# Kernel optimization log

Measured on AMD Instinct MI355X. Metric: run time of the kernel, lower is better.

Reference implementation:

```python
import jax, jax.numpy as jnp
import numpy as np

N, E = 100000, 1600000
IN_C, HID, OUT = 128, 64, 25
EPS = 1e-5


def gcn_conv(x, row, col, W, b):
    # PyG GCNConv: h = x@W; add self-loops; sym-norm D^-1/2 A D^-1/2; + bias
    h = x @ W                                   # [N, F]
    ones = jnp.ones(row.shape[0], h.dtype)
    deg = jax.ops.segment_sum(ones, col, num_segments=N) + 1.0  # +1 self-loop
    dinv = jax.lax.rsqrt(deg)                   # [N]
    norm = dinv[row] * dinv[col]                # [E]
    agg = jax.ops.segment_sum(h[row] * norm[:, None], col, num_segments=N)
    agg = agg + (dinv * dinv)[:, None] * h      # self-loop contribution
    return agg + b


def layer_norm(x, w, b):
    # PyG LayerNorm mode='node': normalize each node over feature dim
    mu = jnp.mean(x, axis=-1, keepdims=True)
    var = jnp.var(x, axis=-1, keepdims=True)
    return (x - mu) * jax.lax.rsqrt(var + EPS) * w + b


def setup_inputs() -> dict:
    key = jax.random.key(0)
    ks = jax.random.split(key, 16)
    x = jax.random.normal(ks[0], (N, IN_C), dtype=jnp.float32)
    edge_index = jax.random.randint(ks[1], (2, E), 0, N, dtype=jnp.int32)

    def glorot(k, shp):
        lim = float(np.sqrt(6.0 / (shp[0] + shp[1])))
        return jax.random.uniform(k, shp, jnp.float32, -lim, lim)

    return {
        "x": x,
        "edge_index": edge_index,
        "W1": glorot(ks[2], (IN_C, HID)), "b1": jnp.zeros((HID,), jnp.float32),
        "W2": glorot(ks[3], (HID, HID)), "b2": jnp.zeros((HID,), jnp.float32),
        "W3": glorot(ks[4], (HID, HID)), "b3": jnp.zeros((HID,), jnp.float32),
        "ln1_w": jnp.ones((HID,), jnp.float32), "ln1_b": jnp.zeros((HID,), jnp.float32),
        "ln2_w": jnp.ones((HID,), jnp.float32), "ln2_b": jnp.zeros((HID,), jnp.float32),
        "ln3_w": jnp.ones((HID,), jnp.float32), "ln3_b": jnp.zeros((HID,), jnp.float32),
        "Wl": glorot(ks[5], (HID, OUT)), "bl": jnp.zeros((OUT,), jnp.float32),
    }


def reference(x, edge_index, W1, b1, W2, b2, W3, b3,
              ln1_w, ln1_b, ln2_w, ln2_b, ln3_w, ln3_b, Wl, bl):
    row, col = edge_index[0], edge_index[1]
    h = jax.nn.relu(layer_norm(gcn_conv(x, row, col, W1, b1), ln1_w, ln1_b))
    h = jax.nn.relu(layer_norm(gcn_conv(h, row, col, W2, b2), ln2_w, ln2_b))
    h = jax.nn.relu(layer_norm(gcn_conv(h, row, col, W3, b3), ln3_w, ln3_b))
    pooled = jnp.mean(h, axis=0)                # [HID]
    return pooled @ Wl + bl                     # [OUT]
```

## Files before the change

### kernel.cpp

```cpp
#include <hip/hip_runtime.h>
#include <hip/hip_bf16.h>

typedef __hip_bfloat16 bf16;
typedef __attribute__((ext_vector_type(8))) short short8;
typedef __attribute__((ext_vector_type(4))) float f32x4;
typedef __attribute__((ext_vector_type(2))) float f32x2;

#define HID 64
#define CAP 4096
#define BSH 7
#define EPB 4096

__device__ __forceinline__ unsigned short f2bfbits(float x){
    union { float f; unsigned u; } c; c.f = x;
    unsigned r = c.u + 0x7fffu + ((c.u >> 16) & 1u);
    return (unsigned short)(r >> 16);
}
__device__ __forceinline__ unsigned char f2fp8(float x){
    unsigned v = __builtin_amdgcn_cvt_pk_fp8_f32(x, x, 0u, false);
    return (unsigned char)(v & 0xffu);
}
template<bool HI>
__device__ __forceinline__ f32x2 cvtpk(unsigned u){
    return __builtin_amdgcn_cvt_pk_f32_fp8(u, HI);
}


__global__ __launch_bounds__(1024) void bin_kernel(const int* __restrict__ row,
                                                   const int* __restrict__ col,
                                                   int E, int NB,
                                                   int* __restrict__ gCur,
                                                   int* __restrict__ cnt,
                                                   int* __restrict__ binned,
                                                   unsigned char* __restrict__ H8a,
                                                   unsigned char* __restrict__ H8b,
                                                   int N){
    __shared__ int lCnt[1024];
    __shared__ int lOff[1024];
    __shared__ int lGB[1024];
    __shared__ int sPay[EPB];
    __shared__ unsigned short sB[EPB];
    __shared__ int wSum[16];
    int tid = threadIdx.x;
    int lane = tid & 63, wv = tid >> 6;
    if (blockIdx.x == 0 && tid < 32){
        unsigned* za = (unsigned*)(H8a + ((size_t)N << 6));
        unsigned* zb = (unsigned*)(H8b + ((size_t)N << 6));
        if (tid < 16) za[tid] = 0u; else zb[tid - 16] = 0u;
    }
    int e0 = blockIdx.x * EPB;
    int eN = E - e0; if (eN > EPB) eN = EPB;

    lCnt[tid] = 0;
    int cols[4], rows[4];
    #pragma unroll
    for (int k = 0; k < 4; ++k){
        int i = tid + k * 1024;
        bool ok = (i < eN);
        cols[k] = ok ? col[e0 + i] : -1;
        rows[k] = ok ? row[e0 + i] : 0;
    }
    #pragma unroll
    for (int k = 0; k < 4; ++k)
        if (cols[k] >= 0) atomicAdd(&cnt[cols[k]], 1);
    __syncthreads();
    #pragma unroll
    for (int k = 0; k < 4; ++k)
        if (cols[k] >= 0) atomicAdd(&lCnt[cols[k] >> BSH], 1);
    __syncthreads();

    int c = lCnt[tid];
    int inc = c;
    #pragma unroll
    for (int m = 1; m < 64; m <<= 1){
        int t = __shfl_up(inc, m);
        if (lane >= m) inc += t;
    }
    if (lane == 63) wSum[wv] = inc;
    __syncthreads();
    if (wv == 0 && lane < 16){
        int orig = wSum[lane];
        int ws = orig;
        #pragma unroll
        for (int m = 1; m < 16; m <<= 1){
            int t = __shfl_up(ws, m);
            if (lane >= m) ws += t;
        }
        wSum[lane] = ws - orig;
    }
    __syncthreads();
    int excl = inc - c + wSum[wv];
    lOff[tid] = excl;
    if (c){
        int gb = atomicAdd(&gCur[tid], c);
        lGB[tid] = tid * CAP + gb - excl;
    }
    lCnt[tid] = 0;
    __syncthreads();

    #pragma unroll
    for (int k = 0; k < 4; ++k){
        if (cols[k] >= 0){
            int bk = cols[k] >> BSH;
            int rk = atomicAdd(&lCnt[bk], 1);
            int pos = lOff[bk] + rk;
            sPay[pos] = ((cols[k] & 127) << 17) | rows[k];
            sB[pos] = (unsigned short)bk;
        }
    }
    __syncthreads();

    #pragma unroll
    for (int k = 0; k < 4; ++k){
        int i = tid + k * 1024;
        if (i < eN){
            int bk = sB[i];
            int tgt = lGB[bk] + i;
            if (tgt - (bk << 12) < CAP)
                binned[tgt] = sPay[i];
        }
    }
}


template<int K, typename T>
__global__ __launch_bounds__(256) void matmul_kernel(const T* __restrict__ act,
                                                     const float* __restrict__ W,
                                                     const int* __restrict__ cnt,
                                                     unsigned char* __restrict__ H8, int N){
    constexpr int KS = K / 32;
    constexpr int RB = 2 * K;
    __shared__ __align__(16) short As[128 * K];
    __shared__ __align__(16) short Wt[64 * K];

    int tid = threadIdx.x;
    int nodeBase = blockIdx.x * 128;

    for (int i = tid; i < K * 64; i += 256){
        int k = i >> 6, c = i & 63;
        unsigned short b = f2bfbits(W[i]);
        int byte = c * RB + ((2 * k) ^ ((c & 7) << 4));
        *(short*)((char*)Wt + byte) = (short)b;
    }
    constexpr int OPR = K / 8;
    for (int i = tid; i < 128 * OPR; i += 256){
        int node = i / OPR, oct = i % OPR;
        int n = nodeBase + node;
        short8 v = (short8)0;
        if (n < N){
            if constexpr (sizeof(T) == 4){
                const float4* xp = (const float4*)&act[(size_t)n * K + oct * 8];
                float4 a = xp[0], b = xp[1];
                v[0] = (short)f2bfbits(a.x); v[1] = (short)f2bfbits(a.y);
                v[2] = (short)f2bfbits(a.z); v[3] = (short)f2bfbits(a.w);
                v[4] = (short)f2bfbits(b.x); v[5] = (short)f2bfbits(b.y);
                v[6] = (short)f2bfbits(b.z); v[7] = (short)f2bfbits(b.w);
            } else {
                v = *(const short8*)&act[(size_t)n * K + oct * 8];
            }
        }
        int byte = node * RB + ((oct * 16) ^ ((node & 7) << 4));
        *(short8*)((char*)As + byte) = v;
    }
    __syncthreads();

    int wv = tid >> 6, l = tid & 63;
    int lr = l & 15, lg = l >> 4;

    short8 bfr[KS][4];
    #pragma unroll
    for (int ks = 0; ks < KS; ++ks)
        #pragma unroll
        for (int t = 0; t < 4; ++t){
            int c = t * 16 + lr;
            int byte = c * RB + ((ks * 64 + lg * 16) ^ ((c & 7) << 4));
            bfr[ks][t] = *(const short8*)((const char*)Wt + byte);
        }

    #pragma unroll
    for (int nt = 0; nt < 2; ++nt){
        int nb = wv * 32 + nt * 16;
        int node = nb + lr;
        short8 af[KS];
        #pragma unroll
        for (int ks = 0; ks < KS; ++ks){
            int byte = node * RB + ((ks * 64 + lg * 16) ^ ((node & 7) << 4));
            af[ks] = *(const short8*)((const char*)As + byte);
        }
        f32x4 acc[4] = {(f32x4)0.f, (f32x4)0.f, (f32x4)0.f, (f32x4)0.f};
        #pragma unroll
        for (int ks = 0; ks < KS; ++ks)
            #pragma unroll
            for (int t = 0; t < 4; ++t)
                acc[t] = __builtin_amdgcn_mfma_f32_16x16x32_bf16(af[ks], bfr[ks][t], acc[t], 0, 0, 0);
        #pragma unroll
        for (int r = 0; r < 4; ++r){
            int n = nodeBase + nb + lg * 4 + r;
            if (n < N){
                float dv = rsqrtf((float)cnt[n] + 1.0f);
                #pragma unroll
                for (int t = 0; t < 4; ++t)
                    H8[((size_t)(unsigned)n << 6) + t * 16 + lr] = f2fp8(acc[t][r] * dv);
            }
        }
    }
}


__global__ __launch_bounds__(512) void agg_sort_kernel(const unsigned char* __restrict__ H8in,
                                                       const int* __restrict__ cnt,
                                                       const int* __restrict__ gCur,
                                                       const int* __restrict__ binned,
                                                       int* __restrict__ csr_row,
                                                       int* __restrict__ col_ptr,
                                                       const float* __restrict__ bias,
                                                       const float* __restrict__ lnw,
                                                       const float* __restrict__ lnb,
                                                       const float* __restrict__ Wn,
                                                       unsigned char* __restrict__ H8out,
                                                       int N){
    __shared__ int sCsr[CAP];
    __shared__ __align__(16) short ybuf[8192];
    __shared__ __align__(16) short Wt[4096];
    __shared__ int fineCnt[128];
    __shared__ int fineCur[128];
    __shared__ int sStart[128];
    __shared__ float sdv[128];
    __shared__ int scW[2];
    int b = blockIdx.x, tid = threadIdx.x;
    int wid = tid >> 6, l = tid & 63;
    int g = l >> 2, s = l & 3;
    int nodeBase = b << BSH;
    int n = nodeBase + wid * 16 + g;
    bool valid = (n < N);
    int nc = valid ? n : nodeBase;

    int j0g = b * CAP;
    int cntB = gCur[b];
    if (cntB > CAP) cntB = CAP;

    for (int i = tid; i < 4096; i += 512){
        int k = i >> 6, c = i & 63;
        unsigned short bb = f2bfbits(Wn[i]);
        int byte = c * 128 + ((2 * k) ^ ((c & 7) << 4));
        *(short*)((char*)Wt + byte) = (short)bb;
    }
    if (tid < 128) fineCnt[tid] = 0;
    __syncthreads();

    for (int i = tid; i < cntB; i += 512)
        atomicAdd(&fineCnt[binned[j0g + i] >> 17], 1);
    __syncthreads();

    int cf = 0, inc = 0;
    if (tid < 128){
        cf = fineCnt[tid];
        inc = cf;
        #pragma unroll
        for (int m = 1; m < 64; m <<= 1){
            int t = __shfl_up(inc, m);
            if ((tid & 63) >= m) inc += t;
        }
        if ((tid & 63) == 63) scW[tid >> 6] = inc;
    }
    __syncthreads();
    if (tid < 128){
        int off = (tid >= 64) ? scW[0] : 0;
        int startL = off + inc - cf;
        sStart[tid] = startL;
        fineCur[tid] = startL;
        int node = nodeBase + tid;
        if (node < N) col_ptr[node] = j0g + startL;
    }
    __syncthreads();

    for (int i = tid; i < cntB; i += 512){
        int w = binned[j0g + i];
        int pos = atomicAdd(&fineCur[w >> 17], 1);
        sCsr[pos] = w & 0x1FFFF;
    }
    __syncthreads();
    for (int i = tid; i < cntB; i += 512) csr_row[j0g + i] = sCsr[i];

    int deg = valid ? cnt[nc] : 0;
    int p = sStart[(wid << 4) + g];
    unsigned soff = (unsigned)(s << 4);
    const char* Hb = (const char*)H8in;
    uint4 us = *(const uint4*)(Hb + ((((unsigned)nc) << 6) | soff));

    int mdeg = deg;
    mdeg = max(mdeg, __shfl_xor(mdeg, 4));
    mdeg = max(mdeg, __shfl_xor(mdeg, 8));
    mdeg = max(mdeg, __shfl_xor(mdeg, 16));
    mdeg = max(mdeg, __shfl_xor(mdeg, 32));

    f32x2 a0 = {0.f,0.f}, a1 = {0.f,0.f}, a2 = {0.f,0.f}, a3 = {0.f,0.f};
    f32x2 a4 = {0.f,0.f}, a5 = {0.f,0.f}, a6 = {0.f,0.f}, a7 = {0.f,0.f};
#define ACC4(u) { a0 += cvtpk<false>((u).x); a1 += cvtpk<true>((u).x); \
                  a2 += cvtpk<false>((u).y); a3 += cvtpk<true>((u).y); \
                  a4 += cvtpk<false>((u).z); a5 += cvtpk<true>((u).z); \
                  a6 += cvtpk<false>((u).w); a7 += cvtpk<true>((u).w); }
    for (int i = 0; i < mdeg; i += 4){
        int r0 = (i     < deg) ? sCsr[p + i    ] : N;
        int r1 = (i + 1 < deg) ? sCsr[p + i + 1] : N;
        int r2 = (i + 2 < deg) ? sCsr[p + i + 2] : N;
        int r3 = (i + 3 < deg) ? sCsr[p + i + 3] : N;
        uint4 u0 = *(const uint4*)(Hb + ((((unsigned)r0) << 6) | soff));
        uint4 u1 = *(const uint4*)(Hb + ((((unsigned)r1) << 6) | soff));
        uint4 u2 = *(const uint4*)(Hb + ((((unsigned)r2) << 6) | soff));
        uint4 u3 = *(const uint4*)(Hb + ((((unsigned)r3) << 6) | soff));
        ACC4(u0) ACC4(u1) ACC4(u2) ACC4(u3)
    }
#undef ACC4
    a0 += cvtpk<false>(us.x); a1 += cvtpk<true>(us.x);
    a2 += cvtpk<false>(us.y); a3 += cvtpk<true>(us.y);
    a4 += cvtpk<false>(us.z); a5 += cvtpk<true>(us.z);
    a6 += cvtpk<false>(us.w); a7 += cvtpk<true>(us.w);

    float dv = rsqrtf((float)deg + 1.0f);
    float acc16[16] = { a0.x, a0.y, a1.x, a1.y, a2.x, a2.y, a3.x, a3.y,
                        a4.x, a4.y, a5.x, a5.y, a6.x, a6.y, a7.x, a7.y };
    float v[16], y[16];
    float4 bq[4], wq[4], cq[4];
    #pragma unroll
    for (int q = 0; q < 4; ++q){
        bq[q] = ((const float4*)bias)[(s << 2) + q];
        wq[q] = ((const float4*)lnw)[(s << 2) + q];
        cq[q] = ((const float4*)lnb)[(s << 2) + q];
    }
    #pragma unroll
    for (int j = 0; j < 16; ++j)
        v[j] = fmaf(dv, acc16[j], ((const float*)&bq[j >> 2])[j & 3]);
    float sum = 0.f;
    #pragma unroll
    for (int j = 0; j < 16; ++j) sum += v[j];
    sum += __shfl_xor(sum, 1); sum += __shfl_xor(sum, 2);
    float mu = sum * (1.0f / 64.0f);
    float var = 0.f;
    #pragma unroll
    for (int j = 0; j < 16; ++j){ float d = v[j] - mu; var = fmaf(d, d, var); }
    var += __shfl_xor(var, 1); var += __shfl_xor(var, 2);
    float rstd = rsqrtf(var * (1.0f / 64.0f) + 1e-5f);
    #pragma unroll
    for (int j = 0; j < 16; ++j){
        float d = (v[j] - mu) * rstd;
        y[j] = fmaxf(fmaf(d, ((const float*)&wq[j >> 2])[j & 3],
                             ((const float*)&cq[j >> 2])[j & 3]), 0.0f);
    }

    if (s == 0) sdv[(wid << 4) + g] = dv;
    char* yb = (char*)ybuf;
    int base = (wid << 11) + (g << 7);
    int sw = (g & 7) << 4;
    short8 ya, yz;
    #pragma unroll
    for (int j = 0; j < 8; ++j){ ya[j] = (short)f2bfbits(y[j]); yz[j] = (short)f2bfbits(y[8 + j]); }
    *(short8*)(yb + base + (((s << 5)     ) ^ sw)) = ya;
    *(short8*)(yb + base + (((s << 5) + 16) ^ sw)) = yz;

    int lr = l & 15, lg = l >> 4;
    short8 bfr[2][4];
    #pragma unroll
    for (int ks = 0; ks < 2; ++ks)
        #pragma unroll
        for (int t = 0; t < 4; ++t){
            int c = t * 16 + lr;
            int byte = c * 128 + ((((ks << 2) + lg) << 4) ^ ((c & 7) << 4));
            bfr[ks][t] = *(const short8*)((const char*)Wt + byte);
        }
    short8 af[2];
    #pragma unroll
    for (int ks = 0; ks < 2; ++ks){
        int byte = (wid << 11) + lr * 128 + ((((ks << 2) + lg) << 4) ^ ((lr & 7) << 4));
        af[ks] = *(const short8*)(yb + byte);
    }
    f32x4 acc[4] = {(f32x4)0.f, (f32x4)0.f, (f32x4)0.f, (f32x4)0.f};
    #pragma unroll
    for (int ks = 0; ks < 2; ++ks)
        #pragma unroll
        for (int t = 0; t < 4; ++t)
            acc[t] = __builtin_amdgcn_mfma_f32_16x16x32_bf16(af[ks], bfr[ks][t], acc[t], 0, 0, 0);
    #pragma unroll
    for (int r = 0; r < 4; ++r){
        int nn = nodeBase + (wid << 4) + (lg << 2) + r;
        if (nn < N){
            float dv2 = sdv[(wid << 4) + (lg << 2) + r];
            #pragma unroll
            for (int t = 0; t < 4; ++t)
                H8out[((size_t)(unsigned)nn << 6) + t * 16 + lr] = f2fp8(acc[t][r] * dv2);
        }
    }
}


template<bool POOL>
__global__ __launch_bounds__(256) void agg_kernel(const unsigned char* __restrict__ H8in,
                                                  const int* __restrict__ cnt,
                                                  const int* __restrict__ col_ptr,
                                                  const int* __restrict__ csr_row,
                                                  const float* __restrict__ bias,
                                                  const float* __restrict__ lnw,
                                                  const float* __restrict__ lnb,
                                                  const float* __restrict__ Wn,
                                                  unsigned char* __restrict__ H8out,
                                                  float* __restrict__ pooledRep, int N){
    __shared__ int sIdx[CAP];
    __shared__ __align__(16) short ybuf[POOL ? 8 : 4096];
    __shared__ __align__(16) short Wt[POOL ? 8 : 4096];
    __shared__ float sp[POOL ? 256 : 4];
    __shared__ float sdv[64];
    int tid = threadIdx.x;
    int wid = tid >> 6, l = tid & 63;
    int g = l >> 2, s = l & 3;
    int nodeBase = blockIdx.x * 64;
    int n = nodeBase + wid * 16 + g;
    bool valid = (n < N);
    int nc = valid ? n : nodeBase;

    int lastN = nodeBase + 63; if (lastN > N - 1) lastN = N - 1;
    int jlo = col_ptr[nodeBase];
    int jhi = col_ptr[lastN] + cnt[lastN];
    int cntR = jhi - jlo;

    int deg = valid ? cnt[nc] : 0;
    int p = (valid ? col_ptr[nc] : jlo) - jlo;

    for (int i = tid; i < cntR; i += 256) sIdx[i] = csr_row[jlo + i];
    if (!POOL){
        for (int i = tid; i < 4096; i += 256){
            int k = i >> 6, c = i & 63;
            unsigned short bb = f2bfbits(Wn[i]);
            int byte = c * 128 + ((2 * k) ^ ((c & 7) << 4));
            *(short*)((char*)Wt + byte) = (short)bb;
        }
    }
    __syncthreads();

    unsigned soff = (unsigned)(s << 4);
    const char* Hb = (const char*)H8in;
    uint4 us = *(const uint4*)(Hb + ((((unsigned)nc) << 6) | soff));

    int mdeg = deg;
    mdeg = max(mdeg, __shfl_xor(mdeg, 4));
    mdeg = max(mdeg, __shfl_xor(mdeg, 8));
    mdeg = max(mdeg, __shfl_xor(mdeg, 16));
    mdeg = max(mdeg, __shfl_xor(mdeg, 32));

    f32x2 a0 = {0.f,0.f}, a1 = {0.f,0.f}, a2 = {0.f,0.f}, a3 = {0.f,0.f};
    f32x2 a4 = {0.f,0.f}, a5 = {0.f,0.f}, a6 = {0.f,0.f}, a7 = {0.f,0.f};
#define ACC4(u) { a0 += cvtpk<false>((u).x); a1 += cvtpk<true>((u).x); \
                  a2 += cvtpk<false>((u).y); a3 += cvtpk<true>((u).y); \
                  a4 += cvtpk<false>((u).z); a5 += cvtpk<true>((u).z); \
                  a6 += cvtpk<false>((u).w); a7 += cvtpk<true>((u).w); }
    for (int i = 0; i < mdeg; i += 4){
        int r0 = (i     < deg) ? sIdx[p + i    ] : N;
        int r1 = (i + 1 < deg) ? sIdx[p + i + 1] : N;
        int r2 = (i + 2 < deg) ? sIdx[p + i + 2] : N;
        int r3 = (i + 3 < deg) ? sIdx[p + i + 3] : N;
        uint4 u0 = *(const uint4*)(Hb + ((((unsigned)r0) << 6) | soff));
        uint4 u1 = *(const uint4*)(Hb + ((((unsigned)r1) << 6) | soff));
        uint4 u2 = *(const uint4*)(Hb + ((((unsigned)r2) << 6) | soff));
        uint4 u3 = *(const uint4*)(Hb + ((((unsigned)r3) << 6) | soff));
        ACC4(u0) ACC4(u1) ACC4(u2) ACC4(u3)
    }
#undef ACC4
    a0 += cvtpk<false>(us.x); a1 += cvtpk<true>(us.x);
    a2 += cvtpk<false>(us.y); a3 += cvtpk<true>(us.y);
    a4 += cvtpk<false>(us.z); a5 += cvtpk<true>(us.z);
    a6 += cvtpk<false>(us.w); a7 += cvtpk<true>(us.w);

    float dv = rsqrtf((float)deg + 1.0f);
    float acc16[16] = { a0.x, a0.y, a1.x, a1.y, a2.x, a2.y, a3.x, a3.y,
                        a4.x, a4.y, a5.x, a5.y, a6.x, a6.y, a7.x, a7.y };
    float v[16], y[16];
    float4 bq[4], wq[4], cq[4];
    #pragma unroll
    for (int q = 0; q < 4; ++q){
        bq[q] = ((const float4*)bias)[(s << 2) + q];
        wq[q] = ((const float4*)lnw)[(s << 2) + q];
        cq[q] = ((const float4*)lnb)[(s << 2) + q];
    }
    #pragma unroll
    for (int j = 0; j < 16; ++j)
        v[j] = fmaf(dv, acc16[j], ((const float*)&bq[j >> 2])[j & 3]);
    float sum = 0.f;
    #pragma unroll
    for (int j = 0; j < 16; ++j) sum += v[j];
    sum += __shfl_xor(sum, 1); sum += __shfl_xor(sum, 2);
    float mu = sum * (1.0f / 64.0f);
    float var = 0.f;
    #pragma unroll
    for (int j = 0; j < 16; ++j){ float d = v[j] - mu; var = fmaf(d, d, var); }
    var += __shfl_xor(var, 1); var += __shfl_xor(var, 2);
    float rstd = rsqrtf(var * (1.0f / 64.0f) + 1e-5f);
    #pragma unroll
    for (int j = 0; j < 16; ++j){
        float d = (v[j] - mu) * rstd;
        y[j] = fmaxf(fmaf(d, ((const float*)&wq[j >> 2])[j & 3],
                             ((const float*)&cq[j >> 2])[j & 3]), 0.0f);
    }

    if (POOL){
        #pragma unroll
        for (int j = 0; j < 16; ++j){
            float z = valid ? y[j] : 0.f;
            z += __shfl_xor(z, 4); z += __shfl_xor(z, 8);
            z += __shfl_xor(z, 16); z += __shfl_xor(z, 32);
            y[j] = z;
        }
        if (l < 4){
            #pragma unroll
            for (int q = 0; q < 4; ++q)
                ((float4*)sp)[wid * 16 + (s << 2) + q] =
                    make_float4(y[4*q], y[4*q+1], y[4*q+2], y[4*q+3]);
        }
        __syncthreads();
        if (tid < 64){
            float t = sp[tid] + sp[64 + tid] + sp[128 + tid] + sp[192 + tid];
            atomicAdd(&pooledRep[(blockIdx.x & 63) * 64 + tid], t);
        }
    } else {
        if (s == 0) sdv[(wid << 4) + g] = dv;
        char* yb = (char*)ybuf;
        int base = (wid << 11) + (g << 7);
        int sw = (g & 7) << 4;
        short8 ya, yz;
        #pragma unroll
        for (int j = 0; j < 8; ++j){ ya[j] = (short)f2bfbits(y[j]); yz[j] = (short)f2bfbits(y[8 + j]); }
        *(short8*)(yb + base + (((s << 5)     ) ^ sw)) = ya;
        *(short8*)(yb + base + (((s << 5) + 16) ^ sw)) = yz;

        int lr = l & 15, lg = l >> 4;
        short8 bfr[2][4];
        #pragma unroll
        for (int ks = 0; ks < 2; ++ks)
            #pragma unroll
            for (int t = 0; t < 4; ++t){
                int c = t * 16 + lr;
                int byte = c * 128 + ((((ks << 2) + lg) << 4) ^ ((c & 7) << 4));
                bfr[ks][t] = *(const short8*)((const char*)Wt + byte);
            }
        short8 af[2];
        #pragma unroll
        for (int ks = 0; ks < 2; ++ks){
            int byte = (wid << 11) + lr * 128 + ((((ks << 2) + lg) << 4) ^ ((lr & 7) << 4));
            af[ks] = *(const short8*)(yb + byte);
        }
        f32x4 acc[4] = {(f32x4)0.f, (f32x4)0.f, (f32x4)0.f, (f32x4)0.f};
        #pragma unroll
        for (int ks = 0; ks < 2; ++ks)
            #pragma unroll
            for (int t = 0; t < 4; ++t)
                acc[t] = __builtin_amdgcn_mfma_f32_16x16x32_bf16(af[ks], bfr[ks][t], acc[t], 0, 0, 0);
        #pragma unroll
        for (int r = 0; r < 4; ++r){
            int nn = nodeBase + (wid << 4) + (lg << 2) + r;
            if (nn < N){
                float dv2 = sdv[(wid << 4) + (lg << 2) + r];
                #pragma unroll
                for (int t = 0; t < 4; ++t)
                    H8out[((size_t)(unsigned)nn << 6) + t * 16 + lr] = f2fp8(acc[t][r] * dv2);
            }
        }
    }
}


__global__ __launch_bounds__(64) void final_kernel(const float* __restrict__ pooledRep,
                                                   const float* __restrict__ Wl,
                                                   const float* __restrict__ bl,
                                                   float* __restrict__ outp, float invN){
    __shared__ float pooled[64];
    int t = threadIdx.x;
    float s = 0.f;
    #pragma unroll 8
    for (int r = 0; r < 64; ++r) s += pooledRep[r * 64 + t];
    pooled[t] = s;
    __syncthreads();
    if (t < 25){
        float acc = bl[t];
        #pragma unroll 8
        for (int f = 0; f < HID; ++f)
            acc = fmaf(pooled[f] * invN, Wl[f * 25 + t], acc);
        outp[t] = acc;
    }
}


static inline size_t alignup(size_t x){ return (x + 255) & ~(size_t)255; }

extern "C" void kernel_launch(void* const* d_in, const int* in_sizes, int n_in,
                              void* d_out, int out_size, void* d_ws, size_t ws_size,
                              hipStream_t stream) {
    const float* x   = (const float*)d_in[0];
    const int*   ei  = (const int*)d_in[1];
    const float* W1  = (const float*)d_in[2];
    const float* b1  = (const float*)d_in[3];
    const float* W2  = (const float*)d_in[4];
    const float* b2  = (const float*)d_in[5];
    const float* W3  = (const float*)d_in[6];
    const float* b3  = (const float*)d_in[7];
    const float* ln1w = (const float*)d_in[8];
    const float* ln1b = (const float*)d_in[9];
    const float* ln2w = (const float*)d_in[10];
    const float* ln2b = (const float*)d_in[11];
    const float* ln3w = (const float*)d_in[12];
    const float* ln3b = (const float*)d_in[13];
    const float* Wl  = (const float*)d_in[14];
    const float* bl  = (const float*)d_in[15];

    const int N = in_sizes[0] / 128;
    const int E = in_sizes[1] / 2;
    const int NB = (N + 127) >> BSH;
    const int* row = ei;
    const int* col = ei + E;

    char* p = (char*)d_ws;
    int*   gCur      = (int*)p;   p += alignup((size_t)NB * 4);
    int*   cnt       = (int*)p;   p += alignup((size_t)N * 4);
    float* pooledRep = (float*)p; p += alignup(64 * 64 * 4);
    size_t zeroBytes = (size_t)((char*)p - (char*)gCur);
    int*   binned    = (int*)p;   p += alignup((size_t)NB * CAP * 4);
    int*   csr_row   = (int*)p;   p += alignup((size_t)NB * CAP * 4);
    int*   col_ptr   = (int*)p;   p += alignup((size_t)N * 4);
    unsigned char* H8a = (unsigned char*)p; p += alignup(((size_t)N + 1) * HID);
    unsigned char* H8b = (unsigned char*)p; p += alignup(((size_t)N + 1) * HID);

    hipMemsetAsync(gCur, 0, zeroBytes, stream);

    int gB = (E + EPB - 1) / EPB;
    int gM = (N + 127) / 128;
    int gA = (N + 63) / 64;

    bin_kernel<<<gB, 1024, 0, stream>>>(row, col, E, NB, gCur, cnt, binned, H8a, H8b, N);

    matmul_kernel<128, float><<<gM, 256, 0, stream>>>(x, W1, cnt, H8a, N);
    agg_sort_kernel<<<NB, 512, 0, stream>>>(H8a, cnt, gCur, binned, csr_row, col_ptr,
                                            b1, ln1w, ln1b, W2, H8b, N);
    agg_kernel<false><<<gA, 256, 0, stream>>>(H8b, cnt, col_ptr, csr_row,
                                              b2, ln2w, ln2b, W3, H8a, pooledRep, N);
    agg_kernel<true><<<gA, 256, 0, stream>>>(H8a, cnt, col_ptr, csr_row,
                                             b3, ln3w, ln3b, nullptr, nullptr, pooledRep, N);

    final_kernel<<<1, 64, 0, stream>>>(pooledRep, Wl, bl, (float*)d_out, 1.0f / (float)N);
}
```

Before: 289.7 us.

## Compute node degrees from binned edges instead of global atomics

Removes the per-edge global atomicAdd on the degree array in the binning kernel. A new per-bucket kernel counts degrees and computes col_ptr from the binned payloads in shared memory, and the aggregation-sort kernel now reads those values instead of recomputing them. Edges per binning block are halved so more blocks run in parallel. The cost is an extra kernel launch and a second read of the binned array, and the cnt buffer no longer needs zeroing.

```diff
diff --git a/kernel.cpp b/kernel.cpp
--- a/kernel.cpp
+++ b/kernel.cpp
@@ -9,7 +9,7 @@
 #define HID 64
 #define CAP 4096
 #define BSH 7
-#define EPB 4096
+#define EPB 2048
 
 __device__ __forceinline__ unsigned short f2bfbits(float x){
     union { float f; unsigned u; } c; c.f = x;
@@ -30,7 +30,6 @@
                                                    const int* __restrict__ col,
                                                    int E, int NB,
                                                    int* __restrict__ gCur,
-                                                   int* __restrict__ cnt,
                                                    int* __restrict__ binned,
                                                    unsigned char* __restrict__ H8a,
                                                    unsigned char* __restrict__ H8b,
@@ -52,20 +51,17 @@
     int eN = E - e0; if (eN > EPB) eN = EPB;
 
     lCnt[tid] = 0;
-    int cols[4], rows[4];
-    #pragma unroll
-    for (int k = 0; k < 4; ++k){
+    int cols[2], rows[2];
+    #pragma unroll
+    for (int k = 0; k < 2; ++k){
         int i = tid + k * 1024;
         bool ok = (i < eN);
         cols[k] = ok ? col[e0 + i] : -1;
         rows[k] = ok ? row[e0 + i] : 0;
     }
-    #pragma unroll
-    for (int k = 0; k < 4; ++k)
-        if (cols[k] >= 0) atomicAdd(&cnt[cols[k]], 1);
-    __syncthreads();
-    #pragma unroll
-    for (int k = 0; k < 4; ++k)
+    __syncthreads();
+    #pragma unroll
+    for (int k = 0; k < 2; ++k)
         if (cols[k] >= 0) atomicAdd(&lCnt[cols[k] >> BSH], 1);
     __syncthreads();
 
@@ -99,7 +95,7 @@
     __syncthreads();
 
     #pragma unroll
-    for (int k = 0; k < 4; ++k){
+    for (int k = 0; k < 2; ++k){
         if (cols[k] >= 0){
             int bk = cols[k] >> BSH;
             int rk = atomicAdd(&lCnt[bk], 1);
@@ -111,13 +107,51 @@
     __syncthreads();
 
     #pragma unroll
-    for (int k = 0; k < 4; ++k){
+    for (int k = 0; k < 2; ++k){
         int i = tid + k * 1024;
         if (i < eN){
             int bk = sB[i];
             int tgt = lGB[bk] + i;
             if (tgt - (bk << 12) < CAP)
                 binned[tgt] = sPay[i];
+        }
+    }
+}
+
+
+__global__ __launch_bounds__(256) void degree_kernel(const int* __restrict__ gCur,
+                                                     const int* __restrict__ binned,
+                                                     int* __restrict__ col_ptr,
+                                                     int* __restrict__ cnt, int N){
+    __shared__ int fineCnt[128];
+    __shared__ int scW[2];
+    int b = blockIdx.x, tid = threadIdx.x;
+    int j0 = b * CAP;
+    int c = gCur[b];
+    if (c > CAP) c = CAP;
+    if (tid < 128) fineCnt[tid] = 0;
+    __syncthreads();
+    for (int i = tid; i < c; i += 256)
+        atomicAdd(&fineCnt[binned[j0 + i] >> 17], 1);
+    __syncthreads();
+    int cf = 0, inc = 0;
+    if (tid < 128){
+        cf = fineCnt[tid];
+        inc = cf;
+        #pragma unroll
+        for (int m = 1; m < 64; m <<= 1){
+            int t = __shfl_up(inc, m);
+            if ((tid & 63) >= m) inc += t;
+        }
+        if ((tid & 63) == 63) scW[tid >> 6] = inc;
+    }
+    __syncthreads();
+    if (tid < 128){
+        int off = (tid >= 64) ? scW[0] : 0;
+        int node = (b << BSH) + tid;
+        if (node < N){
+            col_ptr[node] = j0 + off + inc - cf;
+            cnt[node] = cf;
         }
     }
 }
@@ -211,8 +245,8 @@
                                                        const int* __restrict__ cnt,
                                                        const int* __restrict__ gCur,
                                                        const int* __restrict__ binned,
+                                                       const int* __restrict__ col_ptr,
                                                        int* __restrict__ csr_row,
-                                                       int* __restrict__ col_ptr,
                                                        const float* __restrict__ bias,
                                                        const float* __restrict__ lnw,
                                                        const float* __restrict__ lnb,
@@ -222,11 +256,8 @@
     __shared__ int sCsr[CAP];
     __shared__ __align__(16) short ybuf[8192];
     __shared__ __align__(16) short Wt[4096];
-    __shared__ int fineCnt[128];
     __shared__ int fineCur[128];
-    __shared__ int sStart[128];
     __shared__ float sdv[128];
-    __shared__ int scW[2];
     int b = blockIdx.x, tid = threadIdx.x;
     int wid = tid >> 6, l = tid & 63;
     int g = l >> 2, s = l & 3;
@@ -245,32 +276,9 @@
         int byte = c * 128 + ((2 * k) ^ ((c & 7) << 4));
         *(short*)((char*)Wt + byte) = (short)bb;
     }
-    if (tid < 128) fineCnt[tid] = 0;
-    __syncthreads();
-
-    for (int i = tid; i < cntB; i += 512)
-        atomicAdd(&fineCnt[binned[j0g + i] >> 17], 1);
-    __syncthreads();
-
-    int cf = 0, inc = 0;
     if (tid < 128){
-        cf = fineCnt[tid];
-        inc = cf;
-        #pragma unroll
-        for (int m = 1; m < 64; m <<= 1){
-            int t = __shfl_up(inc, m);
-            if ((tid & 63) >= m) inc += t;
-        }
-        if ((tid & 63) == 63) scW[tid >> 6] = inc;
-    }
-    __syncthreads();
-    if (tid < 128){
-        int off = (tid >= 64) ? scW[0] : 0;
-        int startL = off + inc - cf;
-        sStart[tid] = startL;
-        fineCur[tid] = startL;
         int node = nodeBase + tid;
-        if (node < N) col_ptr[node] = j0g + startL;
+        fineCur[tid] = (node < N) ? (col_ptr[node] - j0g) : 0;
     }
     __syncthreads();
 
@@ -283,7 +291,7 @@
     for (int i = tid; i < cntB; i += 512) csr_row[j0g + i] = sCsr[i];
 
     int deg = valid ? cnt[nc] : 0;
-    int p = sStart[(wid << 4) + g];
+    int p = valid ? (col_ptr[nc] - j0g) : 0;
     unsigned soff = (unsigned)(s << 4);
     const char* Hb = (const char*)H8in;
     uint4 us = *(const uint4*)(Hb + ((((unsigned)nc) << 6) | soff));
@@ -617,12 +625,12 @@
 
     char* p = (char*)d_ws;
     int*   gCur      = (int*)p;   p += alignup((size_t)NB * 4);
-    int*   cnt       = (int*)p;   p += alignup((size_t)N * 4);
     float* pooledRep = (float*)p; p += alignup(64 * 64 * 4);
     size_t zeroBytes = (size_t)((char*)p - (char*)gCur);
     int*   binned    = (int*)p;   p += alignup((size_t)NB * CAP * 4);
     int*   csr_row   = (int*)p;   p += alignup((size_t)NB * CAP * 4);
     int*   col_ptr   = (int*)p;   p += alignup((size_t)N * 4);
+    int*   cnt       = (int*)p;   p += alignup((size_t)N * 4);
     unsigned char* H8a = (unsigned char*)p; p += alignup(((size_t)N + 1) * HID);
     unsigned char* H8b = (unsigned char*)p; p += alignup(((size_t)N + 1) * HID);
 
@@ -632,10 +640,11 @@
     int gM = (N + 127) / 128;
     int gA = (N + 63) / 64;
 
-    bin_kernel<<<gB, 1024, 0, stream>>>(row, col, E, NB, gCur, cnt, binned, H8a, H8b, N);
+    bin_kernel<<<gB, 1024, 0, stream>>>(row, col, E, NB, gCur, binned, H8a, H8b, N);
+    degree_kernel<<<NB, 256, 0, stream>>>(gCur, binned, col_ptr, cnt, N);
 
     matmul_kernel<128, float><<<gM, 256, 0, stream>>>(x, W1, cnt, H8a, N);
-    agg_sort_kernel<<<NB, 512, 0, stream>>>(H8a, cnt, gCur, binned, csr_row, col_ptr,
+    agg_sort_kernel<<<NB, 512, 0, stream>>>(H8a, cnt, gCur, binned, col_ptr, csr_row,
                                             b1, ln1w, ln1b, W2, H8b, N);
     agg_kernel<false><<<gA, 256, 0, stream>>>(H8b, cnt, col_ptr, csr_row,
                                               b2, ln2w, ln2b, W3, H8a, pooledRep, N);
```

Measured after the change: 239.4 us. 17.4% less time.
